# Performance work log

Measured on AMD Instinct MI355X. Metric: run time of the kernel, lower is better.

The kernel has to match this reference:

```python
import jax, jax.numpy as jnp
import numpy as np


def setup_inputs() -> dict:
    key = jax.random.key(0)
    ks = jax.random.split(key, 8)
    N, T, U = 8, 512, 64
    E, D, J, V = 512, 512, 512, 500
    s = 0.02
    return {
        "encoder_out": jax.random.normal(ks[0], (N, T, E), jnp.float32),
        "decoder_out": jax.random.normal(ks[1], (N, U, D), jnp.float32),
        "W_enc": jax.random.normal(ks[2], (J, E), jnp.float32) * s,
        "b_enc": jnp.zeros((J,), jnp.float32),
        "W_dec": jax.random.normal(ks[3], (J, D), jnp.float32) * s,
        "b_dec": jnp.zeros((J,), jnp.float32),
        "W_out": jax.random.normal(ks[4], (V, J), jnp.float32) * s,
        "b_out": jnp.zeros((V,), jnp.float32),
    }


def reference(encoder_out, decoder_out, W_enc, b_enc, W_dec, b_dec, W_out, b_out):
    # Project encoder [N,T,E]->[N,T,J] and decoder [N,U,D]->[N,U,J]
    enc = jnp.einsum("nte,je->ntj", encoder_out, W_enc) + b_enc
    dec = jnp.einsum("nud,jd->nuj", decoder_out, W_dec) + b_dec
    # Broadcast add over (T,U), tanh, then vocab projection -> [N,T,U,V]
    activations = jnp.tanh(enc[:, :, None, :] + dec[:, None, :, :])
    logits = jnp.einsum("ntuj,vj->ntuv", activations, W_out) + b_out
    return logits
```

## Files before the change

### kernel.cpp

```cpp
#include <hip/hip_runtime.h>
#include <hip/hip_bf16.h>


typedef __attribute__((ext_vector_type(4))) float f32x4;
typedef __attribute__((ext_vector_type(16))) float f32x16;
typedef __attribute__((ext_vector_type(4))) short s16x4;
typedef __attribute__((ext_vector_type(8))) short s16x8;
typedef __attribute__((ext_vector_type(4))) unsigned short u16x4;

static __device__ __forceinline__ unsigned short f2bf(float x) {
    union { float f; unsigned u; } v; v.f = x;
    return (unsigned short)((v.u + 0x7FFFu + ((v.u >> 16) & 1u)) >> 16);
}

static __device__ __forceinline__ float bf2f(unsigned short u) {
    union { unsigned u; float f; } v; v.u = ((unsigned)u) << 16;
    return v.f;
}

static __device__ __forceinline__ float fast_tanh(float x) {
    float e = __expf(2.0f * x);
    float r = __builtin_amdgcn_rcpf(e + 1.0f);
    return __builtin_fmaf(-2.0f, r, 1.0f);
}

static __device__ __forceinline__ void lbar() {
    asm volatile("s_waitcnt lgkmcnt(0)" ::: "memory");
    __builtin_amdgcn_s_barrier();
    __builtin_amdgcn_sched_barrier(0);
}

static __device__ __forceinline__ unsigned swz64(int r, int c) {
    return (unsigned)(r * 64 + ((c ^ ((r >> 1) & 3)) << 4));
}

static __device__ void proj_body(
    const float* __restrict__ A, const float* __restrict__ W,
    const float* __restrict__ b, unsigned short* __restrict__ C,
    int mt, int jt, unsigned short* As, unsigned short* Bs)
{
    const int tid = threadIdx.x;
    const int lane = tid & 63, wid = tid >> 6;
    const int wm = wid >> 1, wn = wid & 1;

    f32x4 acc[4][4];
    const f32x4 zero = {0.f, 0.f, 0.f, 0.f};
    #pragma unroll
    for (int i = 0; i < 4; ++i)
        #pragma unroll
        for (int j = 0; j < 4; ++j) acc[i][j] = zero;

    const int c8 = (tid & 7) * 8;
    const int rbase = tid >> 3;

    for (int kt = 0; kt < 8; ++kt) {
        __syncthreads();
        #pragma unroll
        for (int p = 0; p < 4; ++p) {
            int r = p * 32 + rbase;
            int byte = (r * 128 + c8 * 2) ^ ((r & 7) << 4);
            {
                const float* s = A + (size_t)(mt * 128 + r) * 512 + kt * 64 + c8;
                f32x4 v0 = *(const f32x4*)s, v1 = *(const f32x4*)(s + 4);
                s16x8 pk;
                pk[0] = (short)f2bf(v0[0]); pk[1] = (short)f2bf(v0[1]);
                pk[2] = (short)f2bf(v0[2]); pk[3] = (short)f2bf(v0[3]);
                pk[4] = (short)f2bf(v1[0]); pk[5] = (short)f2bf(v1[1]);
                pk[6] = (short)f2bf(v1[2]); pk[7] = (short)f2bf(v1[3]);
                *(s16x8*)((char*)As + byte) = pk;
            }
            {
                const float* s = W + (size_t)(jt * 128 + r) * 512 + kt * 64 + c8;
                f32x4 v0 = *(const f32x4*)s, v1 = *(const f32x4*)(s + 4);
                s16x8 pk;
                pk[0] = (short)f2bf(v0[0]); pk[1] = (short)f2bf(v0[1]);
                pk[2] = (short)f2bf(v0[2]); pk[3] = (short)f2bf(v0[3]);
                pk[4] = (short)f2bf(v1[0]); pk[5] = (short)f2bf(v1[1]);
                pk[6] = (short)f2bf(v1[2]); pk[7] = (short)f2bf(v1[3]);
                *(s16x8*)((char*)Bs + byte) = pk;
            }
        }
        __syncthreads();
        #pragma unroll
        for (int kk = 0; kk < 2; ++kk) {
            s16x8 af[4], bfr[4];
            #pragma unroll
            for (int mi = 0; mi < 4; ++mi) {
                int row = wm * 64 + mi * 16 + (lane & 15);
                int byte = (row * 128 + kk * 64 + ((lane >> 4) * 16)) ^ ((row & 7) << 4);
                af[mi] = *(const s16x8*)((const char*)As + byte);
            }
            #pragma unroll
            for (int ni = 0; ni < 4; ++ni) {
                int row = wn * 64 + ni * 16 + (lane & 15);
                int byte = (row * 128 + kk * 64 + ((lane >> 4) * 16)) ^ ((row & 7) << 4);
                bfr[ni] = *(const s16x8*)((const char*)Bs + byte);
            }
            #pragma unroll
            for (int mi = 0; mi < 4; ++mi)
                #pragma unroll
                for (int ni = 0; ni < 4; ++ni)
                    acc[mi][ni] = __builtin_amdgcn_mfma_f32_16x16x32_bf16(
                        af[mi], bfr[ni], acc[mi][ni], 0, 0, 0);
        }
    }

    #pragma unroll
    for (int ni = 0; ni < 4; ++ni) {
        int col = jt * 128 + wn * 64 + ni * 16 + (lane & 15);
        float bias = b[col];
        #pragma unroll
        for (int mi = 0; mi < 4; ++mi) {
            int row0 = mt * 128 + wm * 64 + mi * 16 + ((lane >> 4) << 2);
            #pragma unroll
            for (int j = 0; j < 4; ++j)
                C[(size_t)(row0 + j) * 512 + col] = f2bf(acc[mi][ni][j] + bias);
        }
    }
}

__global__ __launch_bounds__(256) void prep(
    const float* __restrict__ Wout, unsigned short* __restrict__ img,
    const float* __restrict__ encoder_out, const float* __restrict__ W_enc,
    const float* __restrict__ b_enc, unsigned short* __restrict__ enc_p,
    const float* __restrict__ decoder_out, const float* __restrict__ W_dec,
    const float* __restrict__ b_dec, unsigned short* __restrict__ dec_p,
    const float* __restrict__ b_out, float* __restrict__ bpad)
{
    __shared__ unsigned short As[128 * 64];
    __shared__ unsigned short Bs[128 * 64];
    const int b = blockIdx.x;
    if (b < 128) {
        int tid = b * 256 + threadIdx.x;
        int lane = tid & 63;
        int khalf = (tid >> 6) & 1;
        int tile = (tid >> 7) & 15;
        int kt = tid >> 11;
        int v = tile * 32 + (lane & 31);
        int k = kt * 32 + khalf * 16 + (lane >> 5) * 8;
        s16x8 pk = {0, 0, 0, 0, 0, 0, 0, 0};
        if (v < 500) {
            const float* s = Wout + (size_t)v * 512 + k;
            f32x4 a = *(const f32x4*)s, c = *(const f32x4*)(s + 4);
            pk[0] = (short)f2bf(a[0]); pk[1] = (short)f2bf(a[1]);
            pk[2] = (short)f2bf(a[2]); pk[3] = (short)f2bf(a[3]);
            pk[4] = (short)f2bf(c[0]); pk[5] = (short)f2bf(c[1]);
            pk[6] = (short)f2bf(c[2]); pk[7] = (short)f2bf(c[3]);
        }
        *(s16x8*)(img + (size_t)tid * 8) = pk;
    } else if (b < 256) {
        int q = b - 128;
        proj_body(encoder_out, W_enc, b_enc, enc_p, q & 31, q >> 5, As, Bs);
    } else if (b < 272) {
        int q = b - 256;
        proj_body(decoder_out, W_dec, b_dec, dec_p, q & 3, q >> 2, As, Bs);
    } else {
        int i = threadIdx.x;
        bpad[i] = (i < 500) ? b_out[i] : 0.f;
        bpad[i + 256] = (i + 256 < 500) ? b_out[i + 256] : 0.f;
    }
}

__global__ __launch_bounds__(512, 4) void joiner_main(
    const unsigned short* __restrict__ enc, const unsigned short* __restrict__ dec,
    const unsigned short* __restrict__ Wimg, const float* __restrict__ bout,
    float* __restrict__ out)
{
    __shared__ __align__(16) char raw[66048];
    unsigned short* As0 = (unsigned short*)raw;
    unsigned short* As1 = (unsigned short*)(raw + 4096);
    float* ep = (float*)raw;

    const int bid = blockIdx.x;
    const int tid = threadIdx.x, lane = tid & 63, wn = tid >> 6;
    const int n = bid >> 9, t = bid & 511;

    f32x16 acc[2][2];
    #pragma unroll
    for (int i = 0; i < 2; ++i)
        #pragma unroll
        for (int j = 0; j < 2; ++j)
            #pragma unroll
            for (int e = 0; e < 16; ++e) acc[i][j][e] = 0.f;

    const int r = tid >> 3;
    const int q = tid & 7;
    const unsigned short* erow = enc + ((size_t)n * 512 + t) * 512 + q * 4;
    const unsigned short* drow = dec + ((size_t)n * 64 + r) * 512 + q * 4;
    const unsigned abyte = swz64(r, q >> 1) + (q & 1) * 8;
    const char* wbase = (const char*)Wimg + (size_t)wn * 4096 + (size_t)lane * 16;
    const int lr = lane & 31, kg = lane >> 5;

    u16x4 eN, dN;
    s16x8 bc0, bc1, bc2, bc3;
    {
        u16x4 e = *(const u16x4*)erow;
        u16x4 d = *(const u16x4*)drow;
        s16x4 p;
        p[0] = (short)f2bf(fast_tanh(bf2f(e[0]) + bf2f(d[0])));
        p[1] = (short)f2bf(fast_tanh(bf2f(e[1]) + bf2f(d[1])));
        p[2] = (short)f2bf(fast_tanh(bf2f(e[2]) + bf2f(d[2])));
        p[3] = (short)f2bf(fast_tanh(bf2f(e[3]) + bf2f(d[3])));
        *(s16x4*)((char*)As0 + abyte) = p;
        eN = *(const u16x4*)(erow + 32);
        dN = *(const u16x4*)(drow + 32);
        bc0 = *(const s16x8*)(wbase);
        bc1 = *(const s16x8*)(wbase + 1024);
        bc2 = *(const s16x8*)(wbase + 2048);
        bc3 = *(const s16x8*)(wbase + 3072);
    }
    lbar();

    #pragma unroll
    for (int kt = 0; kt < 16; ++kt) {
        const char* Ac = (char*)((kt & 1) ? As1 : As0);
        char* An = (char*)((kt & 1) ? As0 : As1);

        if (kt < 15) {
            s16x4 p;
            p[0] = (short)f2bf(fast_tanh(bf2f(eN[0]) + bf2f(dN[0])));
            p[1] = (short)f2bf(fast_tanh(bf2f(eN[1]) + bf2f(dN[1])));
            p[2] = (short)f2bf(fast_tanh(bf2f(eN[2]) + bf2f(dN[2])));
            p[3] = (short)f2bf(fast_tanh(bf2f(eN[3]) + bf2f(dN[3])));
            *(s16x4*)(An + abyte) = p;
        }
        if (kt < 14) {
            eN = *(const u16x4*)(erow + (kt + 2) * 32);
            dN = *(const u16x4*)(drow + (kt + 2) * 32);
        }
        s16x8 bn0, bn1, bn2, bn3;
        if (kt < 15) {
            const char* g = wbase + (size_t)(kt + 1) * 32768;
            bn0 = *(const s16x8*)(g);
            bn1 = *(const s16x8*)(g + 1024);
            bn2 = *(const s16x8*)(g + 2048);
            bn3 = *(const s16x8*)(g + 3072);
        }
        {
            s16x8 a0 = *(const s16x8*)(Ac + swz64(lr, kg));
            s16x8 a1 = *(const s16x8*)(Ac + swz64(32 + lr, kg));
            acc[0][0] = __builtin_amdgcn_mfma_f32_32x32x16_bf16(bc0, a0, acc[0][0], 0, 0, 0);
            acc[0][1] = __builtin_amdgcn_mfma_f32_32x32x16_bf16(bc2, a0, acc[0][1], 0, 0, 0);
            acc[1][0] = __builtin_amdgcn_mfma_f32_32x32x16_bf16(bc0, a1, acc[1][0], 0, 0, 0);
            acc[1][1] = __builtin_amdgcn_mfma_f32_32x32x16_bf16(bc2, a1, acc[1][1], 0, 0, 0);
        }
        {
            s16x8 a0 = *(const s16x8*)(Ac + swz64(lr, 2 + kg));
            s16x8 a1 = *(const s16x8*)(Ac + swz64(32 + lr, 2 + kg));
            acc[0][0] = __builtin_amdgcn_mfma_f32_32x32x16_bf16(bc1, a0, acc[0][0], 0, 0, 0);
            acc[0][1] = __builtin_amdgcn_mfma_f32_32x32x16_bf16(bc3, a0, acc[0][1], 0, 0, 0);
            acc[1][0] = __builtin_amdgcn_mfma_f32_32x32x16_bf16(bc1, a1, acc[1][0], 0, 0, 0);
            acc[1][1] = __builtin_amdgcn_mfma_f32_32x32x16_bf16(bc3, a1, acc[1][1], 0, 0, 0);
        }
        lbar();
        bc0 = bn0; bc1 = bn1; bc2 = bn2; bc3 = bn3;
    }

    const int hi4 = (lane >> 5) * 4;
    #pragma unroll
    for (int o = 0; o < 2; ++o) {
        if (o) lbar();
        {
            const int mi = o;
            #pragma unroll
            for (int ni = 0; ni < 2; ++ni) {
                #pragma unroll
                for (int qq = 0; qq < 4; ++qq) {
                    int v4 = wn * 64 + ni * 32 + qq * 8 + hi4;
                    if (v4 < 500) {
                        f32x4 b = *(const f32x4*)(bout + v4);
                        f32x4 ov;
                        ov[0] = acc[mi][ni][qq * 4 + 0] + b[0];
                        ov[1] = acc[mi][ni][qq * 4 + 1] + b[1];
                        ov[2] = acc[mi][ni][qq * 4 + 2] + b[2];
                        ov[3] = acc[mi][ni][qq * 4 + 3] + b[3];
                        *(f32x4*)(ep + lr * 516 + v4) = ov;
                    }
                }
            }
        }
        lbar();
        const size_t obase = ((size_t)bid * 64 + o * 32) * 500;
        #pragma unroll
        for (int i = 0; i < 8; ++i) {
            int idx = i * 512 + tid;
            if (idx < 4000) {
                int rr = idx / 125;
                int vi = (idx - rr * 125) * 4;
                f32x4 ov = *(const f32x4*)(ep + rr * 516 + vi);
                __builtin_nontemporal_store(ov, (f32x4*)(out + obase + (size_t)idx * 4));
            }
        }
    }
}

extern "C" void kernel_launch(void* const* d_in, const int* in_sizes, int n_in,
                              void* d_out, int out_size, void* d_ws, size_t ws_size,
                              hipStream_t stream) {
    const float* encoder_out = (const float*)d_in[0];
    const float* decoder_out = (const float*)d_in[1];
    const float* W_enc = (const float*)d_in[2];
    const float* b_enc = (const float*)d_in[3];
    const float* W_dec = (const float*)d_in[4];
    const float* b_dec = (const float*)d_in[5];
    const float* W_out = (const float*)d_in[6];
    const float* b_out = (const float*)d_in[7];
    float* out = (float*)d_out;

    unsigned short* enc_p = (unsigned short*)d_ws;
    unsigned short* dec_p = enc_p + (size_t)4096 * 512;
    unsigned short* wimg  = dec_p + (size_t)512 * 512;
    float* bpad = (float*)(wimg + 262144);

    prep<<<dim3(273), 256, 0, stream>>>(W_out, wimg,
                                        encoder_out, W_enc, b_enc, enc_p,
                                        decoder_out, W_dec, b_dec, dec_p,
                                        b_out, bpad);
    joiner_main<<<dim3(4096), 512, 0, stream>>>(enc_p, dec_p, wimg, bpad, out);
}
```

Before: 219.5 us.

## Process two K-steps per barrier with a four-deep LDS activation ring

The main loop now handles two K tiles per iteration using four LDS buffers instead of two. That halves the number of workgroup barriers, and each barrier covers twice as much MFMA work. The tanh activations for two future tiles are produced together, and the W fragment loads are interleaved between the two halves. The cost is more registers for the extra prefetched enc/dec/W fragments, which could hurt occupancy at 512 threads with 4 waves per SIMD.

```diff
diff --git a/kernel.cpp b/kernel.cpp
--- a/kernel.cpp
+++ b/kernel.cpp
@@ -167,8 +167,9 @@
     float* __restrict__ out)
 {
     __shared__ __align__(16) char raw[66048];
-    unsigned short* As0 = (unsigned short*)raw;
-    unsigned short* As1 = (unsigned short*)(raw + 4096);
+    unsigned short* Asr[4] = {
+        (unsigned short*)raw, (unsigned short*)(raw + 4096),
+        (unsigned short*)(raw + 8192), (unsigned short*)(raw + 12288)};
     float* ep = (float*)raw;
 
     const int bid = blockIdx.x;
@@ -191,8 +192,9 @@
     const char* wbase = (const char*)Wimg + (size_t)wn * 4096 + (size_t)lane * 16;
     const int lr = lane & 31, kg = lane >> 5;
 
-    u16x4 eN, dN;
+    u16x4 e0r, d0r, e1r, d1r;
     s16x8 bc0, bc1, bc2, bc3;
+
     {
         u16x4 e = *(const u16x4*)erow;
         u16x4 d = *(const u16x4*)drow;
@@ -201,9 +203,18 @@
         p[1] = (short)f2bf(fast_tanh(bf2f(e[1]) + bf2f(d[1])));
         p[2] = (short)f2bf(fast_tanh(bf2f(e[2]) + bf2f(d[2])));
         p[3] = (short)f2bf(fast_tanh(bf2f(e[3]) + bf2f(d[3])));
-        *(s16x4*)((char*)As0 + abyte) = p;
-        eN = *(const u16x4*)(erow + 32);
-        dN = *(const u16x4*)(drow + 32);
+        *(s16x4*)((char*)Asr[0] + abyte) = p;
+        e = *(const u16x4*)(erow + 32);
+        d = *(const u16x4*)(drow + 32);
+        p[0] = (short)f2bf(fast_tanh(bf2f(e[0]) + bf2f(d[0])));
+        p[1] = (short)f2bf(fast_tanh(bf2f(e[1]) + bf2f(d[1])));
+        p[2] = (short)f2bf(fast_tanh(bf2f(e[2]) + bf2f(d[2])));
+        p[3] = (short)f2bf(fast_tanh(bf2f(e[3]) + bf2f(d[3])));
+        *(s16x4*)((char*)Asr[1] + abyte) = p;
+        e0r = *(const u16x4*)(erow + 2 * 32);
+        d0r = *(const u16x4*)(drow + 2 * 32);
+        e1r = *(const u16x4*)(erow + 3 * 32);
+        d1r = *(const u16x4*)(drow + 3 * 32);
         bc0 = *(const s16x8*)(wbase);
         bc1 = *(const s16x8*)(wbase + 1024);
         bc2 = *(const s16x8*)(wbase + 2048);
@@ -212,48 +223,76 @@
     lbar();
 
     #pragma unroll
-    for (int kt = 0; kt < 16; ++kt) {
-        const char* Ac = (char*)((kt & 1) ? As1 : As0);
-        char* An = (char*)((kt & 1) ? As0 : As1);
-
-        if (kt < 15) {
+    for (int j = 0; j < 8; ++j) {
+        const int kt0 = 2 * j, kt1 = 2 * j + 1;
+        const char* Ac0 = (const char*)Asr[kt0 & 3];
+        const char* Ac1 = (const char*)Asr[kt1 & 3];
+        char* An0 = (char*)Asr[(kt0 + 2) & 3];
+        char* An1 = (char*)Asr[(kt1 + 2) & 3];
+
+        if (j < 7) {
             s16x4 p;
-            p[0] = (short)f2bf(fast_tanh(bf2f(eN[0]) + bf2f(dN[0])));
-            p[1] = (short)f2bf(fast_tanh(bf2f(eN[1]) + bf2f(dN[1])));
-            p[2] = (short)f2bf(fast_tanh(bf2f(eN[2]) + bf2f(dN[2])));
-            p[3] = (short)f2bf(fast_tanh(bf2f(eN[3]) + bf2f(dN[3])));
-            *(s16x4*)(An + abyte) = p;
-        }
-        if (kt < 14) {
-            eN = *(const u16x4*)(erow + (kt + 2) * 32);
-            dN = *(const u16x4*)(drow + (kt + 2) * 32);
+            p[0] = (short)f2bf(fast_tanh(bf2f(e0r[0]) + bf2f(d0r[0])));
+            p[1] = (short)f2bf(fast_tanh(bf2f(e0r[1]) + bf2f(d0r[1])));
+            p[2] = (short)f2bf(fast_tanh(bf2f(e0r[2]) + bf2f(d0r[2])));
+            p[3] = (short)f2bf(fast_tanh(bf2f(e0r[3]) + bf2f(d0r[3])));
+            *(s16x4*)(An0 + abyte) = p;
+            p[0] = (short)f2bf(fast_tanh(bf2f(e1r[0]) + bf2f(d1r[0])));
+            p[1] = (short)f2bf(fast_tanh(bf2f(e1r[1]) + bf2f(d1r[1])));
+            p[2] = (short)f2bf(fast_tanh(bf2f(e1r[2]) + bf2f(d1r[2])));
+            p[3] = (short)f2bf(fast_tanh(bf2f(e1r[3]) + bf2f(d1r[3])));
+            *(s16x4*)(An1 + abyte) = p;
+        }
+        if (j < 6) {
+            e0r = *(const u16x4*)(erow + (kt0 + 4) * 32);
+            d0r = *(const u16x4*)(drow + (kt0 + 4) * 32);
+            e1r = *(const u16x4*)(erow + (kt1 + 4) * 32);
+            d1r = *(const u16x4*)(drow + (kt1 + 4) * 32);
         }
         s16x8 bn0, bn1, bn2, bn3;
-        if (kt < 15) {
-            const char* g = wbase + (size_t)(kt + 1) * 32768;
+        {
+            const char* g = wbase + (size_t)kt1 * 32768;
             bn0 = *(const s16x8*)(g);
             bn1 = *(const s16x8*)(g + 1024);
             bn2 = *(const s16x8*)(g + 2048);
             bn3 = *(const s16x8*)(g + 3072);
         }
         {
-            s16x8 a0 = *(const s16x8*)(Ac + swz64(lr, kg));
-            s16x8 a1 = *(const s16x8*)(Ac + swz64(32 + lr, kg));
+            s16x8 a0 = *(const s16x8*)(Ac0 + swz64(lr, kg));
+            s16x8 a1 = *(const s16x8*)(Ac0 + swz64(32 + lr, kg));
             acc[0][0] = __builtin_amdgcn_mfma_f32_32x32x16_bf16(bc0, a0, acc[0][0], 0, 0, 0);
             acc[0][1] = __builtin_amdgcn_mfma_f32_32x32x16_bf16(bc2, a0, acc[0][1], 0, 0, 0);
             acc[1][0] = __builtin_amdgcn_mfma_f32_32x32x16_bf16(bc0, a1, acc[1][0], 0, 0, 0);
             acc[1][1] = __builtin_amdgcn_mfma_f32_32x32x16_bf16(bc2, a1, acc[1][1], 0, 0, 0);
-        }
-        {
-            s16x8 a0 = *(const s16x8*)(Ac + swz64(lr, 2 + kg));
-            s16x8 a1 = *(const s16x8*)(Ac + swz64(32 + lr, 2 + kg));
+            a0 = *(const s16x8*)(Ac0 + swz64(lr, 2 + kg));
+            a1 = *(const s16x8*)(Ac0 + swz64(32 + lr, 2 + kg));
             acc[0][0] = __builtin_amdgcn_mfma_f32_32x32x16_bf16(bc1, a0, acc[0][0], 0, 0, 0);
             acc[0][1] = __builtin_amdgcn_mfma_f32_32x32x16_bf16(bc3, a0, acc[0][1], 0, 0, 0);
             acc[1][0] = __builtin_amdgcn_mfma_f32_32x32x16_bf16(bc1, a1, acc[1][0], 0, 0, 0);
             acc[1][1] = __builtin_amdgcn_mfma_f32_32x32x16_bf16(bc3, a1, acc[1][1], 0, 0, 0);
         }
+        if (j < 7) {
+            const char* g = wbase + (size_t)(kt0 + 2) * 32768;
+            bc0 = *(const s16x8*)(g);
+            bc1 = *(const s16x8*)(g + 1024);
+            bc2 = *(const s16x8*)(g + 2048);
+            bc3 = *(const s16x8*)(g + 3072);
+        }
+        {
+            s16x8 a0 = *(const s16x8*)(Ac1 + swz64(lr, kg));
+            s16x8 a1 = *(const s16x8*)(Ac1 + swz64(32 + lr, kg));
+            acc[0][0] = __builtin_amdgcn_mfma_f32_32x32x16_bf16(bn0, a0, acc[0][0], 0, 0, 0);
+            acc[0][1] = __builtin_amdgcn_mfma_f32_32x32x16_bf16(bn2, a0, acc[0][1], 0, 0, 0);
+            acc[1][0] = __builtin_amdgcn_mfma_f32_32x32x16_bf16(bn0, a1, acc[1][0], 0, 0, 0);
+            acc[1][1] = __builtin_amdgcn_mfma_f32_32x32x16_bf16(bn2, a1, acc[1][1], 0, 0, 0);
+            a0 = *(const s16x8*)(Ac1 + swz64(lr, 2 + kg));
+            a1 = *(const s16x8*)(Ac1 + swz64(32 + lr, 2 + kg));
+            acc[0][0] = __builtin_amdgcn_mfma_f32_32x32x16_bf16(bn1, a0, acc[0][0], 0, 0, 0);
+            acc[0][1] = __builtin_amdgcn_mfma_f32_32x32x16_bf16(bn3, a0, acc[0][1], 0, 0, 0);
+            acc[1][0] = __builtin_amdgcn_mfma_f32_32x32x16_bf16(bn1, a1, acc[1][0], 0, 0, 0);
+            acc[1][1] = __builtin_amdgcn_mfma_f32_32x32x16_bf16(bn3, a1, acc[1][1], 0, 0, 0);
+        }
         lbar();
-        bc0 = bn0; bc1 = bn1; bc2 = bn2; bc3 = bn3;
     }
 
     const int hi4 = (lane >> 5) * 4;
```

New measurement: 219.2 us. No clear change (-0.1%).

## Split vocab across two 256-thread blocks and shrink epilogue LDS staging

Applied to the files above, without the earlier changes.

The main joiner kernel now splits the vocab dimension across two blocks of 256 threads, with 8192 blocks instead of 4096 blocks of 512. The epilogue stages 16-row chunks in a much smaller LDS buffer, which should allow more resident blocks per CU. Activation tiles are now built with 8-wide loads, and the tanh computation moves after the MFMAs to overlap with matrix work. The cost is that each block recomputes the full tanh activation tile for its vocab half, doubling that elementwise work, and the epilogue needs more barriers.

```diff
diff --git a/kernel.cpp b/kernel.cpp
--- a/kernel.cpp
+++ b/kernel.cpp
@@ -6,7 +6,7 @@
 typedef __attribute__((ext_vector_type(16))) float f32x16;
 typedef __attribute__((ext_vector_type(4))) short s16x4;
 typedef __attribute__((ext_vector_type(8))) short s16x8;
-typedef __attribute__((ext_vector_type(4))) unsigned short u16x4;
+typedef __attribute__((ext_vector_type(8))) unsigned short u16x8;
 
 static __device__ __forceinline__ unsigned short f2bf(float x) {
     union { float f; unsigned u; } v; v.f = x;
@@ -161,19 +161,19 @@
     }
 }
 
-__global__ __launch_bounds__(512, 4) void joiner_main(
+__global__ __launch_bounds__(256, 4) void joiner_main(
     const unsigned short* __restrict__ enc, const unsigned short* __restrict__ dec,
     const unsigned short* __restrict__ Wimg, const float* __restrict__ bout,
     float* __restrict__ out)
 {
-    __shared__ __align__(16) char raw[66048];
+    __shared__ __align__(16) char raw[8192 + 16 * 260 * 4];
     unsigned short* As0 = (unsigned short*)raw;
     unsigned short* As1 = (unsigned short*)(raw + 4096);
-    float* ep = (float*)raw;
+    float* ep = (float*)(raw + 8192);
 
     const int bid = blockIdx.x;
     const int tid = threadIdx.x, lane = tid & 63, wn = tid >> 6;
-    const int n = bid >> 9, t = bid & 511;
+    const int vt = bid & 1, t = (bid >> 1) & 511, n = bid >> 10;
 
     f32x16 acc[2][2];
     #pragma unroll
@@ -183,27 +183,24 @@
             #pragma unroll
             for (int e = 0; e < 16; ++e) acc[i][j][e] = 0.f;
 
-    const int r = tid >> 3;
-    const int q = tid & 7;
-    const unsigned short* erow = enc + ((size_t)n * 512 + t) * 512 + q * 4;
-    const unsigned short* drow = dec + ((size_t)n * 64 + r) * 512 + q * 4;
-    const unsigned abyte = swz64(r, q >> 1) + (q & 1) * 8;
-    const char* wbase = (const char*)Wimg + (size_t)wn * 4096 + (size_t)lane * 16;
+    const int r = tid >> 2;
+    const int q = tid & 3;
+    const unsigned short* erow = enc + ((size_t)n * 512 + t) * 512 + q * 8;
+    const unsigned short* drow = dec + ((size_t)n * 64 + r) * 512 + q * 8;
+    const unsigned abyte = swz64(r, q);
+    const char* wbase = (const char*)Wimg + (size_t)(vt * 8 + wn * 2) * 2048
+                        + (size_t)lane * 16;
     const int lr = lane & 31, kg = lane >> 5;
 
-    u16x4 eN, dN;
     s16x8 bc0, bc1, bc2, bc3;
     {
-        u16x4 e = *(const u16x4*)erow;
-        u16x4 d = *(const u16x4*)drow;
-        s16x4 p;
-        p[0] = (short)f2bf(fast_tanh(bf2f(e[0]) + bf2f(d[0])));
-        p[1] = (short)f2bf(fast_tanh(bf2f(e[1]) + bf2f(d[1])));
-        p[2] = (short)f2bf(fast_tanh(bf2f(e[2]) + bf2f(d[2])));
-        p[3] = (short)f2bf(fast_tanh(bf2f(e[3]) + bf2f(d[3])));
-        *(s16x4*)((char*)As0 + abyte) = p;
-        eN = *(const u16x4*)(erow + 32);
-        dN = *(const u16x4*)(drow + 32);
+        u16x8 e = *(const u16x8*)erow;
+        u16x8 d = *(const u16x8*)drow;
+        s16x8 p;
+        #pragma unroll
+        for (int i = 0; i < 8; ++i)
+            p[i] = (short)f2bf(fast_tanh(bf2f(e[i]) + bf2f(d[i])));
+        *(s16x8*)((char*)As0 + abyte) = p;
         bc0 = *(const s16x8*)(wbase);
         bc1 = *(const s16x8*)(wbase + 1024);
         bc2 = *(const s16x8*)(wbase + 2048);
@@ -216,17 +213,10 @@
         const char* Ac = (char*)((kt & 1) ? As1 : As0);
         char* An = (char*)((kt & 1) ? As0 : As1);
 
+        u16x8 eL, dL;
         if (kt < 15) {
-            s16x4 p;
-            p[0] = (short)f2bf(fast_tanh(bf2f(eN[0]) + bf2f(dN[0])));
-            p[1] = (short)f2bf(fast_tanh(bf2f(eN[1]) + bf2f(dN[1])));
-            p[2] = (short)f2bf(fast_tanh(bf2f(eN[2]) + bf2f(dN[2])));
-            p[3] = (short)f2bf(fast_tanh(bf2f(eN[3]) + bf2f(dN[3])));
-            *(s16x4*)(An + abyte) = p;
-        }
-        if (kt < 14) {
-            eN = *(const u16x4*)(erow + (kt + 2) * 32);
-            dN = *(const u16x4*)(drow + (kt + 2) * 32);
+            eL = *(const u16x8*)(erow + (kt + 1) * 32);
+            dL = *(const u16x8*)(drow + (kt + 1) * 32);
         }
         s16x8 bn0, bn1, bn2, bn3;
         if (kt < 15) {
@@ -243,30 +233,38 @@
             acc[0][1] = __builtin_amdgcn_mfma_f32_32x32x16_bf16(bc2, a0, acc[0][1], 0, 0, 0);
             acc[1][0] = __builtin_amdgcn_mfma_f32_32x32x16_bf16(bc0, a1, acc[1][0], 0, 0, 0);
             acc[1][1] = __builtin_amdgcn_mfma_f32_32x32x16_bf16(bc2, a1, acc[1][1], 0, 0, 0);
-        }
-        {
-            s16x8 a0 = *(const s16x8*)(Ac + swz64(lr, 2 + kg));
-            s16x8 a1 = *(const s16x8*)(Ac + swz64(32 + lr, 2 + kg));
+            a0 = *(const s16x8*)(Ac + swz64(lr, 2 + kg));
+            a1 = *(const s16x8*)(Ac + swz64(32 + lr, 2 + kg));
             acc[0][0] = __builtin_amdgcn_mfma_f32_32x32x16_bf16(bc1, a0, acc[0][0], 0, 0, 0);
             acc[0][1] = __builtin_amdgcn_mfma_f32_32x32x16_bf16(bc3, a0, acc[0][1], 0, 0, 0);
             acc[1][0] = __builtin_amdgcn_mfma_f32_32x32x16_bf16(bc1, a1, acc[1][0], 0, 0, 0);
             acc[1][1] = __builtin_amdgcn_mfma_f32_32x32x16_bf16(bc3, a1, acc[1][1], 0, 0, 0);
         }
+        if (kt < 15) {
+            s16x8 p;
+            #pragma unroll
+            for (int i = 0; i < 8; ++i)
+                p[i] = (short)f2bf(fast_tanh(bf2f(eL[i]) + bf2f(dL[i])));
+            *(s16x8*)(An + abyte) = p;
+        }
         lbar();
         bc0 = bn0; bc1 = bn1; bc2 = bn2; bc3 = bn3;
     }
 
-    const int hi4 = (lane >> 5) * 4;
-    #pragma unroll
-    for (int o = 0; o < 2; ++o) {
+    const int hi4 = kg * 4;
+    const size_t mg = ((size_t)n * 512 + t) * 64;
+    #pragma unroll
+    for (int o = 0; o < 4; ++o) {
         if (o) lbar();
-        {
-            const int mi = o;
+        if ((lr >> 4) == (o & 1)) {
+            const int mi = o >> 1;
+            const int lrow = lr & 15;
             #pragma unroll
             for (int ni = 0; ni < 2; ++ni) {
                 #pragma unroll
                 for (int qq = 0; qq < 4; ++qq) {
-                    int v4 = wn * 64 + ni * 32 + qq * 8 + hi4;
+                    int vloc = wn * 64 + ni * 32 + qq * 8 + hi4;
+                    int v4 = vt * 256 + vloc;
                     if (v4 < 500) {
                         f32x4 b = *(const f32x4*)(bout + v4);
                         f32x4 ov;
@@ -274,21 +272,22 @@
                         ov[1] = acc[mi][ni][qq * 4 + 1] + b[1];
                         ov[2] = acc[mi][ni][qq * 4 + 2] + b[2];
                         ov[3] = acc[mi][ni][qq * 4 + 3] + b[3];
-                        *(f32x4*)(ep + lr * 516 + v4) = ov;
+                        *(f32x4*)(ep + lrow * 260 + vloc) = ov;
                     }
                 }
             }
         }
         lbar();
-        const size_t obase = ((size_t)bid * 64 + o * 32) * 500;
-        #pragma unroll
-        for (int i = 0; i < 8; ++i) {
-            int idx = i * 512 + tid;
-            if (idx < 4000) {
-                int rr = idx / 125;
-                int vi = (idx - rr * 125) * 4;
-                f32x4 ov = *(const f32x4*)(ep + rr * 516 + vi);
-                __builtin_nontemporal_store(ov, (f32x4*)(out + obase + (size_t)idx * 4));
+        const int row0 = (o >> 1) * 32 + (o & 1) * 16;
+        #pragma unroll
+        for (int i = 0; i < 4; ++i) {
+            int idx = i * 256 + tid;
+            int rr = idx >> 6, ci = idx & 63;
+            int v4 = vt * 256 + ci * 4;
+            if (v4 < 500) {
+                f32x4 ov = *(const f32x4*)(ep + rr * 260 + ci * 4);
+                __builtin_nontemporal_store(
+                    ov, (f32x4*)(out + (mg + row0 + rr) * 500 + v4));
             }
         }
     }
@@ -316,5 +315,5 @@
                                         encoder_out, W_enc, b_enc, enc_p,
                                         decoder_out, W_dec, b_dec, dec_p,
                                         b_out, bpad);
-    joiner_main<<<dim3(4096), 512, 0, stream>>>(enc_p, dec_p, wimg, bpad, out);
-}
+    joiner_main<<<dim3(8192), 256, 0, stream>>>(enc_p, dec_p, wimg, bpad, out);
+}
```

Result: slower. 266.5 us (+21.4%).

## Make joiner persistent over 16 timesteps and overlap output stores with next GEMM

Applied to the files above, without the earlier changes.

Each block now loops over 16 consecutive t values instead of one, reducing the grid from 4096 to 256 blocks. The epilogue tile gets its own LDS region so the previous timestep's output stores are spread across the next timestep's k-loop iterations, overlapping global writes with MFMA work. Bias values are hoisted into registers once per block. The cost is fewer blocks (256, about one per CU), larger LDS use and lower occupancy via launch bounds, which may limit latency hiding on the store-bound output.

```diff
diff --git a/kernel.cpp b/kernel.cpp
--- a/kernel.cpp
+++ b/kernel.cpp
@@ -161,134 +161,150 @@
     }
 }
 
-__global__ __launch_bounds__(512, 4) void joiner_main(
+__global__ __launch_bounds__(512, 2) void joiner_main(
     const unsigned short* __restrict__ enc, const unsigned short* __restrict__ dec,
     const unsigned short* __restrict__ Wimg, const float* __restrict__ bout,
     float* __restrict__ out)
 {
-    __shared__ __align__(16) char raw[66048];
+    __shared__ __align__(16) char raw[8192 + 64 * 516 * 4];
     unsigned short* As0 = (unsigned short*)raw;
     unsigned short* As1 = (unsigned short*)(raw + 4096);
-    float* ep = (float*)raw;
+    float* ep = (float*)(raw + 8192);
 
     const int bid = blockIdx.x;
     const int tid = threadIdx.x, lane = tid & 63, wn = tid >> 6;
-    const int n = bid >> 9, t = bid & 511;
-
-    f32x16 acc[2][2];
-    #pragma unroll
-    for (int i = 0; i < 2; ++i)
-        #pragma unroll
-        for (int j = 0; j < 2; ++j)
-            #pragma unroll
-            for (int e = 0; e < 16; ++e) acc[i][j][e] = 0.f;
+    const int n = bid >> 5;
+    const int t0 = (bid & 31) * 16;
 
     const int r = tid >> 3;
     const int q = tid & 7;
-    const unsigned short* erow = enc + ((size_t)n * 512 + t) * 512 + q * 4;
     const unsigned short* drow = dec + ((size_t)n * 64 + r) * 512 + q * 4;
     const unsigned abyte = swz64(r, q >> 1) + (q & 1) * 8;
     const char* wbase = (const char*)Wimg + (size_t)wn * 4096 + (size_t)lane * 16;
     const int lr = lane & 31, kg = lane >> 5;
-
-    u16x4 eN, dN;
-    s16x8 bc0, bc1, bc2, bc3;
-    {
-        u16x4 e = *(const u16x4*)erow;
-        u16x4 d = *(const u16x4*)drow;
-        s16x4 p;
-        p[0] = (short)f2bf(fast_tanh(bf2f(e[0]) + bf2f(d[0])));
-        p[1] = (short)f2bf(fast_tanh(bf2f(e[1]) + bf2f(d[1])));
-        p[2] = (short)f2bf(fast_tanh(bf2f(e[2]) + bf2f(d[2])));
-        p[3] = (short)f2bf(fast_tanh(bf2f(e[3]) + bf2f(d[3])));
-        *(s16x4*)((char*)As0 + abyte) = p;
-        eN = *(const u16x4*)(erow + 32);
-        dN = *(const u16x4*)(drow + 32);
-        bc0 = *(const s16x8*)(wbase);
-        bc1 = *(const s16x8*)(wbase + 1024);
-        bc2 = *(const s16x8*)(wbase + 2048);
-        bc3 = *(const s16x8*)(wbase + 3072);
-    }
-    lbar();
-
+    const int hi4 = kg * 4;
+
+    f32x4 brg[2][4];
     #pragma unroll
-    for (int kt = 0; kt < 16; ++kt) {
-        const char* Ac = (char*)((kt & 1) ? As1 : As0);
-        char* An = (char*)((kt & 1) ? As0 : As1);
-
-        if (kt < 15) {
+    for (int ni = 0; ni < 2; ++ni)
+        #pragma unroll
+        for (int qq = 0; qq < 4; ++qq)
+            brg[ni][qq] = *(const f32x4*)(bout + wn * 64 + ni * 32 + qq * 8 + hi4);
+
+    f32x16 acc[2][2];
+
+    for (int j = 0; j < 16; ++j) {
+        const int t = t0 + j;
+        const unsigned short* erow = enc + ((size_t)n * 512 + t) * 512 + q * 4;
+        const size_t pslab = (((size_t)n * 512 + (t - 1)) * 64) * 500;
+
+        #pragma unroll
+        for (int i = 0; i < 2; ++i)
+            #pragma unroll
+            for (int jj = 0; jj < 2; ++jj)
+                #pragma unroll
+                for (int e = 0; e < 16; ++e) acc[i][jj][e] = 0.f;
+
+        u16x4 eN, dN;
+        s16x8 bc0, bc1, bc2, bc3;
+        {
+            u16x4 e = *(const u16x4*)erow;
+            u16x4 d = *(const u16x4*)drow;
             s16x4 p;
-            p[0] = (short)f2bf(fast_tanh(bf2f(eN[0]) + bf2f(dN[0])));
-            p[1] = (short)f2bf(fast_tanh(bf2f(eN[1]) + bf2f(dN[1])));
-            p[2] = (short)f2bf(fast_tanh(bf2f(eN[2]) + bf2f(dN[2])));
-            p[3] = (short)f2bf(fast_tanh(bf2f(eN[3]) + bf2f(dN[3])));
-            *(s16x4*)(An + abyte) = p;
-        }
-        if (kt < 14) {
-            eN = *(const u16x4*)(erow + (kt + 2) * 32);
-            dN = *(const u16x4*)(drow + (kt + 2) * 32);
-        }
-        s16x8 bn0, bn1, bn2, bn3;
-        if (kt < 15) {
-            const char* g = wbase + (size_t)(kt + 1) * 32768;
-            bn0 = *(const s16x8*)(g);
-            bn1 = *(const s16x8*)(g + 1024);
-            bn2 = *(const s16x8*)(g + 2048);
-            bn3 = *(const s16x8*)(g + 3072);
-        }
-        {
-            s16x8 a0 = *(const s16x8*)(Ac + swz64(lr, kg));
-            s16x8 a1 = *(const s16x8*)(Ac + swz64(32 + lr, kg));
-            acc[0][0] = __builtin_amdgcn_mfma_f32_32x32x16_bf16(bc0, a0, acc[0][0], 0, 0, 0);
-            acc[0][1] = __builtin_amdgcn_mfma_f32_32x32x16_bf16(bc2, a0, acc[0][1], 0, 0, 0);
-            acc[1][0] = __builtin_amdgcn_mfma_f32_32x32x16_bf16(bc0, a1, acc[1][0], 0, 0, 0);
-            acc[1][1] = __builtin_amdgcn_mfma_f32_32x32x16_bf16(bc2, a1, acc[1][1], 0, 0, 0);
-        }
-        {
-            s16x8 a0 = *(const s16x8*)(Ac + swz64(lr, 2 + kg));
-            s16x8 a1 = *(const s16x8*)(Ac + swz64(32 + lr, 2 + kg));
-            acc[0][0] = __builtin_amdgcn_mfma_f32_32x32x16_bf16(bc1, a0, acc[0][0], 0, 0, 0);
-            acc[0][1] = __builtin_amdgcn_mfma_f32_32x32x16_bf16(bc3, a0, acc[0][1], 0, 0, 0);
-            acc[1][0] = __builtin_amdgcn_mfma_f32_32x32x16_bf16(bc1, a1, acc[1][0], 0, 0, 0);
-            acc[1][1] = __builtin_amdgcn_mfma_f32_32x32x16_bf16(bc3, a1, acc[1][1], 0, 0, 0);
+            p[0] = (short)f2bf(fast_tanh(bf2f(e[0]) + bf2f(d[0])));
+            p[1] = (short)f2bf(fast_tanh(bf2f(e[1]) + bf2f(d[1])));
+            p[2] = (short)f2bf(fast_tanh(bf2f(e[2]) + bf2f(d[2])));
+            p[3] = (short)f2bf(fast_tanh(bf2f(e[3]) + bf2f(d[3])));
+            *(s16x4*)((char*)As0 + abyte) = p;
+            eN = *(const u16x4*)(erow + 32);
+            dN = *(const u16x4*)(drow + 32);
+            bc0 = *(const s16x8*)(wbase);
+            bc1 = *(const s16x8*)(wbase + 1024);
+            bc2 = *(const s16x8*)(wbase + 2048);
+            bc3 = *(const s16x8*)(wbase + 3072);
         }
         lbar();
-        bc0 = bn0; bc1 = bn1; bc2 = bn2; bc3 = bn3;
-    }
-
-    const int hi4 = (lane >> 5) * 4;
-    #pragma unroll
-    for (int o = 0; o < 2; ++o) {
-        if (o) lbar();
-        {
-            const int mi = o;
+
+        for (int kt = 0; kt < 16; ++kt) {
+            const char* Ac = (char*)((kt & 1) ? As1 : As0);
+            char* An = (char*)((kt & 1) ? As0 : As1);
+
+            if (kt < 15) {
+                s16x4 p;
+                p[0] = (short)f2bf(fast_tanh(bf2f(eN[0]) + bf2f(dN[0])));
+                p[1] = (short)f2bf(fast_tanh(bf2f(eN[1]) + bf2f(dN[1])));
+                p[2] = (short)f2bf(fast_tanh(bf2f(eN[2]) + bf2f(dN[2])));
+                p[3] = (short)f2bf(fast_tanh(bf2f(eN[3]) + bf2f(dN[3])));
+                *(s16x4*)(An + abyte) = p;
+            }
+            if (kt < 14) {
+                eN = *(const u16x4*)(erow + (kt + 2) * 32);
+                dN = *(const u16x4*)(drow + (kt + 2) * 32);
+            }
+            s16x8 bn0, bn1, bn2, bn3;
+            if (kt < 15) {
+                const char* g = wbase + (size_t)(kt + 1) * 32768;
+                bn0 = *(const s16x8*)(g);
+                bn1 = *(const s16x8*)(g + 1024);
+                bn2 = *(const s16x8*)(g + 2048);
+                bn3 = *(const s16x8*)(g + 3072);
+            }
+            {
+                s16x8 a00 = *(const s16x8*)(Ac + swz64(lr, kg));
+                s16x8 a10 = *(const s16x8*)(Ac + swz64(32 + lr, kg));
+                s16x8 a01 = *(const s16x8*)(Ac + swz64(lr, 2 + kg));
+                s16x8 a11 = *(const s16x8*)(Ac + swz64(32 + lr, 2 + kg));
+                acc[0][0] = __builtin_amdgcn_mfma_f32_32x32x16_bf16(bc0, a00, acc[0][0], 0, 0, 0);
+                acc[0][1] = __builtin_amdgcn_mfma_f32_32x32x16_bf16(bc2, a00, acc[0][1], 0, 0, 0);
+                acc[1][0] = __builtin_amdgcn_mfma_f32_32x32x16_bf16(bc0, a10, acc[1][0], 0, 0, 0);
+                acc[1][1] = __builtin_amdgcn_mfma_f32_32x32x16_bf16(bc2, a10, acc[1][1], 0, 0, 0);
+                acc[0][0] = __builtin_amdgcn_mfma_f32_32x32x16_bf16(bc1, a01, acc[0][0], 0, 0, 0);
+                acc[0][1] = __builtin_amdgcn_mfma_f32_32x32x16_bf16(bc3, a01, acc[0][1], 0, 0, 0);
+                acc[1][0] = __builtin_amdgcn_mfma_f32_32x32x16_bf16(bc1, a11, acc[1][0], 0, 0, 0);
+                acc[1][1] = __builtin_amdgcn_mfma_f32_32x32x16_bf16(bc3, a11, acc[1][1], 0, 0, 0);
+            }
+            if (j > 0 && tid < 500) {
+                int idx = kt * 500 + tid;
+                int rr = idx / 125;
+                int vi = (idx - rr * 125) * 4;
+                f32x4 ov = *(const f32x4*)(ep + rr * 516 + vi);
+                __builtin_nontemporal_store(
+                    ov, (f32x4*)(out + pslab + (size_t)rr * 500 + vi));
+            }
+            lbar();
+            bc0 = bn0; bc1 = bn1; bc2 = bn2; bc3 = bn3;
+        }
+
+        #pragma unroll
+        for (int mi = 0; mi < 2; ++mi) {
             #pragma unroll
             for (int ni = 0; ni < 2; ++ni) {
                 #pragma unroll
                 for (int qq = 0; qq < 4; ++qq) {
                     int v4 = wn * 64 + ni * 32 + qq * 8 + hi4;
-                    if (v4 < 500) {
-                        f32x4 b = *(const f32x4*)(bout + v4);
-                        f32x4 ov;
-                        ov[0] = acc[mi][ni][qq * 4 + 0] + b[0];
-                        ov[1] = acc[mi][ni][qq * 4 + 1] + b[1];
-                        ov[2] = acc[mi][ni][qq * 4 + 2] + b[2];
-                        ov[3] = acc[mi][ni][qq * 4 + 3] + b[3];
-                        *(f32x4*)(ep + lr * 516 + v4) = ov;
-                    }
+                    f32x4 ov;
+                    ov[0] = acc[mi][ni][qq * 4 + 0] + brg[ni][qq][0];
+                    ov[1] = acc[mi][ni][qq * 4 + 1] + brg[ni][qq][1];
+                    ov[2] = acc[mi][ni][qq * 4 + 2] + brg[ni][qq][2];
+                    ov[3] = acc[mi][ni][qq * 4 + 3] + brg[ni][qq][3];
+                    *(f32x4*)(ep + (mi * 32 + lr) * 516 + v4) = ov;
                 }
             }
         }
         lbar();
-        const size_t obase = ((size_t)bid * 64 + o * 32) * 500;
-        #pragma unroll
-        for (int i = 0; i < 8; ++i) {
-            int idx = i * 512 + tid;
-            if (idx < 4000) {
+    }
+
+    {
+        const size_t pslab = (((size_t)n * 512 + (t0 + 15)) * 64) * 500;
+        #pragma unroll
+        for (int kt = 0; kt < 16; ++kt) {
+            if (tid < 500) {
+                int idx = kt * 500 + tid;
                 int rr = idx / 125;
                 int vi = (idx - rr * 125) * 4;
                 f32x4 ov = *(const f32x4*)(ep + rr * 516 + vi);
-                __builtin_nontemporal_store(ov, (f32x4*)(out + obase + (size_t)idx * 4));
+                __builtin_nontemporal_store(
+                    ov, (f32x4*)(out + pslab + (size_t)rr * 500 + vi));
             }
         }
     }
@@ -316,5 +332,5 @@
                                         encoder_out, W_enc, b_enc, enc_p,
                                         decoder_out, W_dec, b_dec, dec_p,
                                         b_out, bpad);
-    joiner_main<<<dim3(4096), 512, 0, stream>>>(enc_p, dec_p, wimg, bpad, out);
-}
+    joiner_main<<<dim3(256), 512, 0, stream>>>(enc_p, dec_p, wimg, bpad, out);
+}
```

Result: slower. 245.5 us (+11.8%).
